# Kernel tuning notes

Hardware: AMD Instinct MI355X
Metric: run time of the kernel (lower is better)

## Reference

```python
import jax, jax.numpy as jnp
import numpy as np
import math

WS = 7  # window size
NUM_HEADS = 6

def _relative_position_index(ws):
    coords = np.stack(np.meshgrid(np.arange(ws), np.arange(ws), indexing='ij'))  # 2,ws,ws
    cf = coords.reshape(2, -1)
    rel = cf[:, :, None] - cf[:, None, :]            # 2,N,N
    rel = rel.transpose(1, 2, 0).astype(np.int64)    # N,N,2
    rel[:, :, 0] += ws - 1
    rel[:, :, 1] += ws - 1
    rel[:, :, 0] *= 2 * ws - 1
    return jnp.asarray(rel.sum(-1))                  # N,N

RPI = _relative_position_index(WS)

def setup_inputs() -> dict:
    key = jax.random.key(0)
    ks = jax.random.split(key, 6)
    C = 192
    return {
        'x': jax.random.normal(ks[0], (32, 3136, C), dtype=jnp.float32),
        'gamma': jnp.ones((C,), dtype=jnp.float32),
        'rpb_table': jax.random.normal(ks[1], (169, NUM_HEADS), dtype=jnp.float32) * 0.02,
        'qkv_w': jax.random.normal(ks[2], (3 * C, C), dtype=jnp.float32) * (1.0 / math.sqrt(C)),
        'qkv_b': jax.random.normal(ks[3], (3 * C,), dtype=jnp.float32) * 0.02,
        'proj_w': jax.random.normal(ks[4], (C, C), dtype=jnp.float32) * (1.0 / math.sqrt(C)),
        'proj_b': jax.random.normal(ks[5], (C,), dtype=jnp.float32) * 0.02,
    }

def reference(x, gamma, rpb_table, qkv_w, qkv_b, proj_w, proj_b):
    B_, N, C = x.shape
    H = W = int(math.isqrt(N))
    h = NUM_HEADS
    d = C // h
    scale = d ** -0.5
    ws = WS
    NW = ws * ws  # tokens per window (49)

    # LayerNorm (beta = 0)
    mu = jnp.mean(x, axis=-1, keepdims=True)
    var = jnp.var(x, axis=-1, keepdims=True)
    xn = (x - mu) * jax.lax.rsqrt(var + 1e-5) * gamma

    # window partition: (B_,H,W,C) -> (B_*nWh*nWw, ws*ws, C)
    xn = xn.reshape(B_, H // ws, ws, W // ws, ws, C)
    xw = xn.transpose(0, 1, 3, 2, 4, 5).reshape(-1, NW, C)
    BW = xw.shape[0]

    # qkv projection
    qkv = xw @ qkv_w.T + qkv_b                        # (BW, NW, 3C)
    qkv = qkv.reshape(BW, NW, 3, h, d).transpose(2, 0, 3, 1, 4)
    q, k, v = qkv[0], qkv[1], qkv[2]                  # (BW, h, NW, d)

    attn = jnp.einsum('bhnd,bhmd->bhnm', q * scale, k)
    bias = rpb_table[RPI.reshape(-1)].reshape(NW, NW, h).transpose(2, 0, 1)
    attn = jax.nn.softmax(attn + bias[None], axis=-1)

    out = jnp.einsum('bhnm,bhmd->bhnd', attn, v)      # (BW, h, NW, d)
    out = out.transpose(0, 2, 1, 3).reshape(BW, NW, C)
    out = out @ proj_w.T + proj_b

    # window reverse
    out = out.reshape(B_, H // ws, W // ws, ws, ws, C)
    out = out.transpose(0, 1, 3, 2, 4, 5).reshape(B_, H * W, C)
    return out
```

## Files before the change

### kernel.cpp

```cpp
#include <hip/hip_runtime.h>


typedef __bf16 bf16x8 __attribute__((ext_vector_type(8)));
typedef float  f32x4  __attribute__((ext_vector_type(4)));
typedef unsigned int u32;
union U128 { uint4 u; bf16x8 v; };

__device__ __forceinline__ f32x4 mfma16(bf16x8 a, bf16x8 b, f32x4 c){
  return __builtin_amdgcn_mfma_f32_16x16x32_bf16(a, b, c, 0, 0, 0);
}
__device__ __forceinline__ f32x4 f4zero(){
  f32x4 z; z[0]=0.f; z[1]=0.f; z[2]=0.f; z[3]=0.f; return z;
}
__device__ __forceinline__ unsigned short f2bf(float f){
  union{float f; unsigned int i;} x; x.f = f;
  unsigned int r = x.i + 0x7fffu + ((x.i >> 16) & 1u);
  return (unsigned short)(r >> 16);
}
__device__ __forceinline__ bf16x8 ldfrag(const unsigned short* p){
  U128 x; x.u = *(const uint4*)p; return x.v;
}
__device__ __forceinline__ int div7(int t){ return (t * 9363) >> 16; }

__device__ __forceinline__ void glds16(const unsigned short* g, unsigned short* l){
  __builtin_amdgcn_global_load_lds((const __attribute__((address_space(1))) u32*)g,
                                   (__attribute__((address_space(3))) u32*)l, 16, 0, 0);
}

__global__ __launch_bounds__(256, 8) void wa_ln(
    const float* __restrict__ x, const float* __restrict__ gamma,
    unsigned short* __restrict__ xng,
    const float* __restrict__ qkv_w, const float* __restrict__ proj_w,
    const float* __restrict__ rpb,
    unsigned short* __restrict__ wq, unsigned short* __restrict__ wp,
    float* __restrict__ bt)
{
  const int tid  = threadIdx.x;

  if (blockIdx.x < 432){
    int i = blockIdx.x * 256 + tid;
    if (i < 576*192) wq[i] = f2bf(qkv_w[i]);
    if (i < 192*192) wp[i] = f2bf(proj_w[i]);
    if (i < 6*64*64){
      int head = i >> 12, t = (i >> 6) & 63, j = i & 63;
      int l16 = j >> 2, nt = j & 3;
      int col = nt*16 + l16;
      float v;
      if (t < 49 && col < 49){
        int tr = div7(t),   tc = t   - tr*7;
        int jr = div7(col), jc = col - jr*7;
        v = rpb[((tr - jr + 6)*13 + (tc - jc + 6))*6 + head];
      } else {
        v = (col >= 49) ? -3.0e38f : 0.0f;
      }
      bt[i] = v;
    }
  }

  const int wave = tid >> 6, lane = tid & 63;
  const int wid  = blockIdx.x * 4 + wave;
  const int wi   = wid >> 6, t = wid & 63;
  unsigned short* dst = xng + (size_t)wid * 192;
  if (t >= 49){
    if (lane < 24){ const uint4 z = {0u,0u,0u,0u}; *(uint4*)&dst[lane*8] = z; }
    return;
  }
  const int b = wi >> 6, wr = (wi >> 3) & 7, wc = wi & 7;
  const int tr = div7(t), tc = t - tr*7;
  const float* xt = x + ((size_t)b*3136 + (size_t)((wr*7 + tr)*56 + wc*7 + tc)) * 192;
  float v0 = xt[lane], v1 = xt[lane+64], v2 = xt[lane+128];
  float s  = v0 + v1 + v2;
  float sq = v0*v0 + v1*v1 + v2*v2;
#pragma unroll
  for (int off = 32; off > 0; off >>= 1){
    s  += __shfl_xor(s,  off);
    sq += __shfl_xor(sq, off);
  }
  float mu  = s * (1.0f/192.0f);
  float var = sq * (1.0f/192.0f) - mu*mu;
  float inv = rsqrtf(var + 1e-5f);
  const int sw = (t & 7) << 3;
  dst[lane        ^ sw] = f2bf((v0 - mu)*inv*gamma[lane]);
  dst[(lane + 64) ^ sw] = f2bf((v1 - mu)*inv*gamma[lane+64]);
  dst[(lane + 128)^ sw] = f2bf((v2 - mu)*inv*gamma[lane+128]);
}

__global__ __launch_bounds__(384, 5) void wa_k1(
    const unsigned short* __restrict__ xng, const float* __restrict__ bt,
    const unsigned short* __restrict__ wq, const float* __restrict__ qkv_b,
    unsigned short* __restrict__ attn)
{
  __shared__ __align__(16) unsigned short qk[3*64*72];
  __shared__ __align__(16) unsigned short xnb[64*192];

  const int p    = blockIdx.x;
  const int blk  = (p & 7) * 512 + (p >> 3);
  const int wi   = blk >> 1;
  const int h0   = (blk & 1) * 3;
  const int b    = wi >> 6;
  const int wr   = (wi >> 3) & 7;
  const int wc   = wi & 7;
  const int tid  = threadIdx.x;
  const int wave = tid >> 6;
  const int lane = tid & 63;
  const int quad = lane >> 4;
  const int l16  = lane & 15;

  {
    const unsigned short* xw = xng + (size_t)wi * 64 * 192;
#pragma unroll
    for (int j = 0; j < 4; j++){
      const int chunk = wave*4 + j;
      glds16(xw + chunk*512 + lane*8, &xnb[chunk*512]);
    }
  }
  __syncthreads();

  f32x4 acc[4][3];
  {
    const int sec = wave >> 1;
    const int n0  = sec*192 + h0*32 + (wave & 1)*48;
#pragma unroll
    for (int mt = 0; mt < 4; mt++)
#pragma unroll
      for (int nt = 0; nt < 3; nt++) acc[mt][nt] = f4zero();

#pragma unroll
    for (int kt = 0; kt < 6; kt++){
      bf16x8 a[4], bw[3];
#pragma unroll
      for (int nt = 0; nt < 3; nt++)
        bw[nt] = ldfrag(&wq[(size_t)(n0 + nt*16 + l16)*192 + kt*32 + quad*8]);
#pragma unroll
      for (int mt = 0; mt < 4; mt++)
        a[mt] = ldfrag(&xnb[(mt*16 + l16)*192 + ((kt*32 + quad*8) ^ ((l16 & 7) << 3))]);
#pragma unroll
      for (int mt = 0; mt < 4; mt++)
#pragma unroll
        for (int nt = 0; nt < 3; nt++)
          acc[mt][nt] = mfma16(a[mt], bw[nt], acc[mt][nt]);
    }
  }
  __syncthreads();

  unsigned short* const vt = xnb;
  {
    const int sec = wave >> 1;
    const int n0  = sec*192 + h0*32 + (wave & 1)*48;
    const float scale = 0.17677669529663687f;
#pragma unroll
    for (int nt = 0; nt < 3; nt++){
      const int bc = (wave & 1)*48 + nt*16 + l16;
      const int hl2 = bc >> 5, d = bc & 31;
      const float bias = qkv_b[n0 + nt*16 + l16];
#pragma unroll
      for (int mt = 0; mt < 4; mt++)
#pragma unroll
        for (int r = 0; r < 4; r++){
          const int row = mt*16 + quad*4 + r;
          const float val = acc[mt][nt][r] + bias;
          if (sec == 0)      qk[(hl2*64 + row)*72 + d]      = f2bf(val * scale);
          else if (sec == 1) qk[(hl2*64 + row)*72 + 32 + d] = f2bf(val);
          else               vt[(hl2*32 + d)*72 + row]      = f2bf(val);
        }
    }
  }
  __syncthreads();

  const int hl   = wave >> 1;
  const int half = wave & 1;
  const int head = h0 + hl;

  f32x4 bias4[2][4];
#pragma unroll
  for (int i = 0; i < 2; i++)
#pragma unroll
    for (int r = 0; r < 4; r++){
      const int t = half*32 + i*16 + quad*4 + r;
      bias4[i][r] = *(const f32x4*)&bt[head*4096 + t*64 + l16*4];
    }

  bf16x8 aq[2];
#pragma unroll
  for (int i = 0; i < 2; i++)
    aq[i] = ldfrag(&qk[(hl*64 + half*32 + i*16 + l16)*72 + quad*8]);

  f32x4 s[2][4];
#pragma unroll
  for (int nt = 0; nt < 4; nt++){
    bf16x8 bk = ldfrag(&qk[(hl*64 + nt*16 + l16)*72 + 32 + quad*8]);
#pragma unroll
    for (int i = 0; i < 2; i++)
      s[i][nt] = mfma16(aq[i], bk, f4zero());
  }

  __syncthreads();

  float linv[2][4];
#pragma unroll
  for (int i = 0; i < 2; i++)
#pragma unroll
    for (int r = 0; r < 4; r++){
      const f32x4 b4 = bias4[i][r];
#pragma unroll
      for (int nt = 0; nt < 4; nt++) s[i][nt][r] += b4[nt];
      float m = fmaxf(fmaxf(s[i][0][r], s[i][1][r]), fmaxf(s[i][2][r], s[i][3][r]));
#pragma unroll
      for (int off = 8; off > 0; off >>= 1) m = fmaxf(m, __shfl_xor(m, off));
      float l = 0.f;
      const int t = half*32 + i*16 + quad*4 + r;
#pragma unroll
      for (int nt = 0; nt < 4; nt++){
        float pexp = __expf(s[i][nt][r] - m);
        l += pexp;
        qk[hl*4608 + t*72 + nt*16 + l16] = f2bf(pexp);
      }
#pragma unroll
      for (int off = 8; off > 0; off >>= 1) l += __shfl_xor(l, off);
      linv[i][r] = 1.f / l;
    }

  f32x4 o[2][2];
#pragma unroll
  for (int i = 0; i < 2; i++)
#pragma unroll
    for (int n2 = 0; n2 < 2; n2++) o[i][n2] = f4zero();
#pragma unroll
  for (int kt = 0; kt < 2; kt++){
    bf16x8 ap[2], bv[2];
#pragma unroll
    for (int i = 0; i < 2; i++)
      ap[i] = ldfrag(&qk[hl*4608 + (half*32 + i*16 + l16)*72 + kt*32 + quad*8]);
#pragma unroll
    for (int n2 = 0; n2 < 2; n2++)
      bv[n2] = ldfrag(&vt[(hl*32 + n2*16 + l16)*72 + kt*32 + quad*8]);
#pragma unroll
    for (int i = 0; i < 2; i++)
#pragma unroll
      for (int n2 = 0; n2 < 2; n2++)
        o[i][n2] = mfma16(ap[i], bv[n2], o[i][n2]);
  }

#pragma unroll
  for (int i = 0; i < 2; i++)
#pragma unroll
    for (int r = 0; r < 4; r++){
      const int t = half*32 + i*16 + quad*4 + r;
      if (t < 49){
        const int tr = div7(t), tcc = t - tr*7;
        const size_t base =
          ((size_t)b*3136 + (size_t)((wr*7 + tr)*56 + wc*7 + tcc))*192 + head*32;
        const float inv = linv[i][r];
        attn[base + l16]      = f2bf(o[i][0][r] * inv);
        attn[base + 16 + l16] = f2bf(o[i][1][r] * inv);
      }
    }
}

__global__ __launch_bounds__(256, 4) void wa_k2(
    const unsigned short* __restrict__ a, const unsigned short* __restrict__ wp,
    const float* __restrict__ pb, float* __restrict__ out)
{
  const int mblk = blockIdx.x;
  const int nblk = blockIdx.y;
  const int tid  = threadIdx.x;
  const int wave = tid >> 6;
  const int lane = tid & 63;
  const int quad = lane >> 4;
  const int l16  = lane & 15;

  bf16x8 av[6][2];
#pragma unroll
  for (int kt = 0; kt < 6; kt++)
#pragma unroll
    for (int i = 0; i < 2; i++)
      av[kt][i] = ldfrag(&a[(size_t)(mblk*128 + (wave*2 + i)*16 + l16)*192 + kt*32 + quad*8]);
  __builtin_amdgcn_sched_barrier(0);

  f32x4 acc[2][4];
#pragma unroll
  for (int i = 0; i < 2; i++)
#pragma unroll
    for (int nt = 0; nt < 4; nt++) acc[i][nt] = f4zero();

#pragma unroll
  for (int kt = 0; kt < 6; kt++){
    bf16x8 bw[4];
#pragma unroll
    for (int nt = 0; nt < 4; nt++)
      bw[nt] = ldfrag(&wp[(size_t)(nblk*64 + nt*16 + l16)*192 + kt*32 + quad*8]);
#pragma unroll
    for (int i = 0; i < 2; i++)
#pragma unroll
      for (int nt = 0; nt < 4; nt++)
        acc[i][nt] = mfma16(av[kt][i], bw[nt], acc[i][nt]);
  }

#pragma unroll
  for (int nt = 0; nt < 4; nt++){
    const int col = nblk*64 + nt*16 + l16;
    const float bias = pb[col];
#pragma unroll
    for (int i = 0; i < 2; i++)
#pragma unroll
      for (int r = 0; r < 4; r++){
        const int row = mblk*128 + (wave*2 + i)*16 + quad*4 + r;
        out[(size_t)row*192 + col] = acc[i][nt][r] + bias;
      }
  }
}

extern "C" void kernel_launch(void* const* d_in, const int* in_sizes, int n_in,
                              void* d_out, int out_size, void* d_ws, size_t ws_size,
                              hipStream_t stream) {
  (void)in_sizes; (void)n_in; (void)out_size; (void)ws_size;
  const float* x      = (const float*)d_in[0];
  const float* gamma  = (const float*)d_in[1];
  const float* rpb    = (const float*)d_in[2];
  const float* qkv_w  = (const float*)d_in[3];
  const float* qkv_b  = (const float*)d_in[4];
  const float* proj_w = (const float*)d_in[5];
  const float* proj_b = (const float*)d_in[6];

  unsigned short* wq   = (unsigned short*)d_ws;
  unsigned short* wp   = wq + 576*192;
  float* bt            = (float*)(wp + 192*192);
  unsigned short* attn = (unsigned short*)(bt + 6*64*64);

  unsigned short* xng = (unsigned short*)d_out;
  float* out = (float*)d_out;

  hipLaunchKernelGGL(wa_ln, dim3(32768), dim3(256), 0, stream,
                     x, gamma, xng, qkv_w, proj_w, rpb, wq, wp, bt);
  hipLaunchKernelGGL(wa_k1, dim3(4096), dim3(384), 0, stream,
                     xng, bt, wq, qkv_b, attn);
  hipLaunchKernelGGL(wa_k2, dim3(784, 3), dim3(256), 0, stream,
                     attn, wp, proj_b, out);
}
```

Measured before the change: 306.0 us.

## Fuse output projection into window attention kernel, one block per window

The attention kernel now processes all six heads of a window in one block. It does them in two rounds of three heads, interleaving the QKV GEMM of the next round with attention. It then applies the output projection on the attention result kept in LDS, so the separate projection kernel and the bf16 attention round-trip through global memory go away. The LayerNorm kernel now runs one block per window and stores the normalized tokens compactly (49 rows) in workspace instead of padded 64 rows in the output buffer, and the attention kernel zero-pads in LDS. This trades more LDS and registers per block and lower occupancy (launch bound 3) for less global traffic and one fewer launch.

```diff
diff --git a/kernel.cpp b/kernel.cpp
--- a/kernel.cpp
+++ b/kernel.cpp
@@ -35,7 +35,7 @@
     unsigned short* __restrict__ wq, unsigned short* __restrict__ wp,
     float* __restrict__ bt)
 {
-  const int tid  = threadIdx.x;
+  const int tid = threadIdx.x;
 
   if (blockIdx.x < 432){
     int i = blockIdx.x * 256 + tid;
@@ -58,45 +58,45 @@
   }
 
   const int wave = tid >> 6, lane = tid & 63;
-  const int wid  = blockIdx.x * 4 + wave;
-  const int wi   = wid >> 6, t = wid & 63;
-  unsigned short* dst = xng + (size_t)wid * 192;
-  if (t >= 49){
-    if (lane < 24){ const uint4 z = {0u,0u,0u,0u}; *(uint4*)&dst[lane*8] = z; }
-    return;
+  const int wi = blockIdx.x;
+  const int b = wi >> 6, wrr = (wi >> 3) & 7, wcc = wi & 7;
+  const float g0 = gamma[lane], g1 = gamma[lane+64], g2 = gamma[lane+128];
+  const float* xb = x + (size_t)b * 3136 * 192;
+
+  for (int t = wave; t < 49; t += 4){
+    const int tr = div7(t), tc = t - tr*7;
+    const float* xt = xb + (size_t)((wrr*7 + tr)*56 + wcc*7 + tc) * 192;
+    float v0 = xt[lane], v1 = xt[lane+64], v2 = xt[lane+128];
+    float s  = v0 + v1 + v2;
+    float sq = v0*v0 + v1*v1 + v2*v2;
+#pragma unroll
+    for (int off = 32; off > 0; off >>= 1){
+      s  += __shfl_xor(s,  off);
+      sq += __shfl_xor(sq, off);
+    }
+    float mu  = s * (1.0f/192.0f);
+    float var = sq * (1.0f/192.0f) - mu*mu;
+    float inv = rsqrtf(var + 1e-5f);
+    unsigned short* dst = xng + ((size_t)wi*49 + t) * 192;
+    const int sw = (t & 7) << 3;
+    dst[lane        ^ sw] = f2bf((v0 - mu)*inv*g0);
+    dst[(lane + 64) ^ sw] = f2bf((v1 - mu)*inv*g1);
+    dst[(lane + 128)^ sw] = f2bf((v2 - mu)*inv*g2);
   }
-  const int b = wi >> 6, wr = (wi >> 3) & 7, wc = wi & 7;
-  const int tr = div7(t), tc = t - tr*7;
-  const float* xt = x + ((size_t)b*3136 + (size_t)((wr*7 + tr)*56 + wc*7 + tc)) * 192;
-  float v0 = xt[lane], v1 = xt[lane+64], v2 = xt[lane+128];
-  float s  = v0 + v1 + v2;
-  float sq = v0*v0 + v1*v1 + v2*v2;
-#pragma unroll
-  for (int off = 32; off > 0; off >>= 1){
-    s  += __shfl_xor(s,  off);
-    sq += __shfl_xor(sq, off);
-  }
-  float mu  = s * (1.0f/192.0f);
-  float var = sq * (1.0f/192.0f) - mu*mu;
-  float inv = rsqrtf(var + 1e-5f);
-  const int sw = (t & 7) << 3;
-  dst[lane        ^ sw] = f2bf((v0 - mu)*inv*gamma[lane]);
-  dst[(lane + 64) ^ sw] = f2bf((v1 - mu)*inv*gamma[lane+64]);
-  dst[(lane + 128)^ sw] = f2bf((v2 - mu)*inv*gamma[lane+128]);
-}
-
-__global__ __launch_bounds__(384, 5) void wa_k1(
+}
+
+#define OBS 104
+__global__ __launch_bounds__(384, 3) void wa_k1(
     const unsigned short* __restrict__ xng, const float* __restrict__ bt,
     const unsigned short* __restrict__ wq, const float* __restrict__ qkv_b,
-    unsigned short* __restrict__ attn)
+    const unsigned short* __restrict__ wp, const float* __restrict__ pb,
+    float* __restrict__ out)
 {
   __shared__ __align__(16) unsigned short qk[3*64*72];
+  __shared__ __align__(16) unsigned short vt[3*32*72];
   __shared__ __align__(16) unsigned short xnb[64*192];
 
-  const int p    = blockIdx.x;
-  const int blk  = (p & 7) * 512 + (p >> 3);
-  const int wi   = blk >> 1;
-  const int h0   = (blk & 1) * 3;
+  const int wi   = blockIdx.x;
   const int b    = wi >> 6;
   const int wr   = (wi >> 3) & 7;
   const int wc   = wi & 7;
@@ -105,26 +105,35 @@
   const int lane = tid & 63;
   const int quad = lane >> 4;
   const int l16  = lane & 15;
-
+  const int sec  = wave >> 1, sub = wave & 1;
+  const int hl   = wave >> 1, half = wave & 1;
+
+  unsigned short* const ob = xnb;
+
+  const float pbv0 = pb[wave*32 + l16];
+  const float pbv1 = pb[wave*32 + 16 + l16];
+
+  const unsigned short* xw = xng + (size_t)wi * 49 * 192;
   {
-    const unsigned short* xw = xng + (size_t)wi * 64 * 192;
-#pragma unroll
-    for (int j = 0; j < 4; j++){
-      const int chunk = wave*4 + j;
+    const uint4 z = {0u,0u,0u,0u};
+    for (int i = tid; i < 360; i += 384) *(uint4*)&xnb[9408 + i*8] = z;
+    uint4 r48;
+    if (tid < 24) r48 = *(const uint4*)(xw + 9216 + tid*8);
+#pragma unroll
+    for (int j = 0; j < 3; j++){
+      const int chunk = wave*3 + j;
       glds16(xw + chunk*512 + lane*8, &xnb[chunk*512]);
     }
+    if (tid < 24) *(uint4*)&xnb[9216 + tid*8] = r48;
   }
   __syncthreads();
 
-  f32x4 acc[4][3];
-  {
-    const int sec = wave >> 1;
-    const int n0  = sec*192 + h0*32 + (wave & 1)*48;
+  auto qkv_gemm = [&](f32x4 (*acc)[3], int np){
+    const int n0 = sec*192 + np*96 + sub*48;
 #pragma unroll
     for (int mt = 0; mt < 4; mt++)
 #pragma unroll
       for (int nt = 0; nt < 3; nt++) acc[mt][nt] = f4zero();
-
 #pragma unroll
     for (int kt = 0; kt < 6; kt++){
       bf16x8 a[4], bw[3];
@@ -140,17 +149,14 @@
         for (int nt = 0; nt < 3; nt++)
           acc[mt][nt] = mfma16(a[mt], bw[nt], acc[mt][nt]);
     }
-  }
-  __syncthreads();
-
-  unsigned short* const vt = xnb;
-  {
-    const int sec = wave >> 1;
-    const int n0  = sec*192 + h0*32 + (wave & 1)*48;
+  };
+
+  auto qkv_epi = [&](f32x4 (*acc)[3], int np){
+    const int n0 = sec*192 + np*96 + sub*48;
     const float scale = 0.17677669529663687f;
 #pragma unroll
     for (int nt = 0; nt < 3; nt++){
-      const int bc = (wave & 1)*48 + nt*16 + l16;
+      const int bc = sub*48 + nt*16 + l16;
       const int hl2 = bc >> 5, d = bc & 31;
       const float bias = qkv_b[n0 + nt*16 + l16];
 #pragma unroll
@@ -164,148 +170,147 @@
           else               vt[(hl2*32 + d)*72 + row]      = f2bf(val);
         }
     }
-  }
-  __syncthreads();
-
-  const int hl   = wave >> 1;
-  const int half = wave & 1;
-  const int head = h0 + hl;
-
-  f32x4 bias4[2][4];
-#pragma unroll
-  for (int i = 0; i < 2; i++)
-#pragma unroll
-    for (int r = 0; r < 4; r++){
-      const int t = half*32 + i*16 + quad*4 + r;
-      bias4[i][r] = *(const f32x4*)&bt[head*4096 + t*64 + l16*4];
-    }
-
-  bf16x8 aq[2];
-#pragma unroll
-  for (int i = 0; i < 2; i++)
-    aq[i] = ldfrag(&qk[(hl*64 + half*32 + i*16 + l16)*72 + quad*8]);
-
-  f32x4 s[2][4];
-#pragma unroll
-  for (int nt = 0; nt < 4; nt++){
-    bf16x8 bk = ldfrag(&qk[(hl*64 + nt*16 + l16)*72 + 32 + quad*8]);
-#pragma unroll
-    for (int i = 0; i < 2; i++)
-      s[i][nt] = mfma16(aq[i], bk, f4zero());
-  }
-
-  __syncthreads();
-
-  float linv[2][4];
-#pragma unroll
-  for (int i = 0; i < 2; i++)
-#pragma unroll
-    for (int r = 0; r < 4; r++){
-      const f32x4 b4 = bias4[i][r];
-#pragma unroll
-      for (int nt = 0; nt < 4; nt++) s[i][nt][r] += b4[nt];
-      float m = fmaxf(fmaxf(s[i][0][r], s[i][1][r]), fmaxf(s[i][2][r], s[i][3][r]));
-#pragma unroll
-      for (int off = 8; off > 0; off >>= 1) m = fmaxf(m, __shfl_xor(m, off));
-      float l = 0.f;
-      const int t = half*32 + i*16 + quad*4 + r;
-#pragma unroll
-      for (int nt = 0; nt < 4; nt++){
-        float pexp = __expf(s[i][nt][r] - m);
-        l += pexp;
-        qk[hl*4608 + t*72 + nt*16 + l16] = f2bf(pexp);
-      }
-#pragma unroll
-      for (int off = 8; off > 0; off >>= 1) l += __shfl_xor(l, off);
-      linv[i][r] = 1.f / l;
-    }
-
-  f32x4 o[2][2];
-#pragma unroll
-  for (int i = 0; i < 2; i++)
-#pragma unroll
-    for (int n2 = 0; n2 < 2; n2++) o[i][n2] = f4zero();
-#pragma unroll
-  for (int kt = 0; kt < 2; kt++){
-    bf16x8 ap[2], bv[2];
-#pragma unroll
-    for (int i = 0; i < 2; i++)
-      ap[i] = ldfrag(&qk[hl*4608 + (half*32 + i*16 + l16)*72 + kt*32 + quad*8]);
-#pragma unroll
-    for (int n2 = 0; n2 < 2; n2++)
-      bv[n2] = ldfrag(&vt[(hl*32 + n2*16 + l16)*72 + kt*32 + quad*8]);
-#pragma unroll
-    for (int i = 0; i < 2; i++)
+  };
+
+  auto attn_round = [&](int np){
+    const int head = np*3 + hl;
+    f32x4 bias4[2][4];
+#pragma unroll
+    for (int i = 0; i < 2; i++)
+#pragma unroll
+      for (int r = 0; r < 4; r++){
+        const int t = half*32 + i*16 + quad*4 + r;
+        bias4[i][r] = *(const f32x4*)&bt[head*4096 + t*64 + l16*4];
+      }
+
+    bf16x8 aq[2];
+#pragma unroll
+    for (int i = 0; i < 2; i++)
+      aq[i] = ldfrag(&qk[(hl*64 + half*32 + i*16 + l16)*72 + quad*8]);
+
+    f32x4 s[2][4];
+#pragma unroll
+    for (int nt = 0; nt < 4; nt++){
+      bf16x8 bk = ldfrag(&qk[(hl*64 + nt*16 + l16)*72 + 32 + quad*8]);
+#pragma unroll
+      for (int i = 0; i < 2; i++)
+        s[i][nt] = mfma16(aq[i], bk, f4zero());
+    }
+
+    __syncthreads();
+
+    float linv[2][4];
+#pragma unroll
+    for (int i = 0; i < 2; i++)
+#pragma unroll
+      for (int r = 0; r < 4; r++){
+        const f32x4 b4 = bias4[i][r];
+#pragma unroll
+        for (int nt = 0; nt < 4; nt++) s[i][nt][r] += b4[nt];
+        float m = fmaxf(fmaxf(s[i][0][r], s[i][1][r]), fmaxf(s[i][2][r], s[i][3][r]));
+#pragma unroll
+        for (int off = 8; off > 0; off >>= 1) m = fmaxf(m, __shfl_xor(m, off));
+        float l = 0.f;
+        const int t = half*32 + i*16 + quad*4 + r;
+#pragma unroll
+        for (int nt = 0; nt < 4; nt++){
+          float pexp = __expf(s[i][nt][r] - m);
+          l += pexp;
+          qk[hl*4608 + t*72 + nt*16 + l16] = f2bf(pexp);
+        }
+#pragma unroll
+        for (int off = 8; off > 0; off >>= 1) l += __shfl_xor(l, off);
+        linv[i][r] = 1.f / l;
+      }
+
+    f32x4 o[2][2];
+#pragma unroll
+    for (int i = 0; i < 2; i++)
+#pragma unroll
+      for (int n2 = 0; n2 < 2; n2++) o[i][n2] = f4zero();
+#pragma unroll
+    for (int kt = 0; kt < 2; kt++){
+      bf16x8 ap[2], bv[2];
+#pragma unroll
+      for (int i = 0; i < 2; i++)
+        ap[i] = ldfrag(&qk[hl*4608 + (half*32 + i*16 + l16)*72 + kt*32 + quad*8]);
 #pragma unroll
       for (int n2 = 0; n2 < 2; n2++)
-        o[i][n2] = mfma16(ap[i], bv[n2], o[i][n2]);
-  }
-
-#pragma unroll
-  for (int i = 0; i < 2; i++)
-#pragma unroll
-    for (int r = 0; r < 4; r++){
-      const int t = half*32 + i*16 + quad*4 + r;
-      if (t < 49){
-        const int tr = div7(t), tcc = t - tr*7;
-        const size_t base =
-          ((size_t)b*3136 + (size_t)((wr*7 + tr)*56 + wc*7 + tcc))*192 + head*32;
+        bv[n2] = ldfrag(&vt[(hl*32 + n2*16 + l16)*72 + kt*32 + quad*8]);
+#pragma unroll
+      for (int i = 0; i < 2; i++)
+#pragma unroll
+        for (int n2 = 0; n2 < 2; n2++)
+          o[i][n2] = mfma16(ap[i], bv[n2], o[i][n2]);
+    }
+
+#pragma unroll
+    for (int i = 0; i < 2; i++)
+#pragma unroll
+      for (int r = 0; r < 4; r++){
+        const int t = half*32 + i*16 + quad*4 + r;
         const float inv = linv[i][r];
-        attn[base + l16]      = f2bf(o[i][0][r] * inv);
-        attn[base + 16 + l16] = f2bf(o[i][1][r] * inv);
-      }
-    }
-}
-
-__global__ __launch_bounds__(256, 4) void wa_k2(
-    const unsigned short* __restrict__ a, const unsigned short* __restrict__ wp,
-    const float* __restrict__ pb, float* __restrict__ out)
-{
-  const int mblk = blockIdx.x;
-  const int nblk = blockIdx.y;
-  const int tid  = threadIdx.x;
-  const int wave = tid >> 6;
-  const int lane = tid & 63;
-  const int quad = lane >> 4;
-  const int l16  = lane & 15;
-
-  bf16x8 av[6][2];
-#pragma unroll
-  for (int kt = 0; kt < 6; kt++)
-#pragma unroll
-    for (int i = 0; i < 2; i++)
-      av[kt][i] = ldfrag(&a[(size_t)(mblk*128 + (wave*2 + i)*16 + l16)*192 + kt*32 + quad*8]);
-  __builtin_amdgcn_sched_barrier(0);
-
-  f32x4 acc[2][4];
-#pragma unroll
-  for (int i = 0; i < 2; i++)
-#pragma unroll
-    for (int nt = 0; nt < 4; nt++) acc[i][nt] = f4zero();
-
-#pragma unroll
-  for (int kt = 0; kt < 6; kt++){
-    bf16x8 bw[4];
-#pragma unroll
-    for (int nt = 0; nt < 4; nt++)
-      bw[nt] = ldfrag(&wp[(size_t)(nblk*64 + nt*16 + l16)*192 + kt*32 + quad*8]);
-#pragma unroll
-    for (int i = 0; i < 2; i++)
-#pragma unroll
-      for (int nt = 0; nt < 4; nt++)
-        acc[i][nt] = mfma16(av[kt][i], bw[nt], acc[i][nt]);
-  }
-
-#pragma unroll
-  for (int nt = 0; nt < 4; nt++){
-    const int col = nblk*64 + nt*16 + l16;
-    const float bias = pb[col];
-#pragma unroll
-    for (int i = 0; i < 2; i++)
+        ob[t*OBS + hl*32 + l16]      = f2bf(o[i][0][r] * inv);
+        ob[t*OBS + hl*32 + 16 + l16] = f2bf(o[i][1][r] * inv);
+      }
+  };
+
+  auto proj_part = [&](f32x4 (*pacc)[2], int np){
+#pragma unroll
+    for (int kt = 0; kt < 3; kt++){
+      bf16x8 a2[4], bw2[2];
+#pragma unroll
+      for (int n2 = 0; n2 < 2; n2++)
+        bw2[n2] = ldfrag(&wp[(size_t)(wave*32 + n2*16 + l16)*192 + np*96 + kt*32 + quad*8]);
+#pragma unroll
+      for (int mt = 0; mt < 4; mt++)
+        a2[mt] = ldfrag(&ob[(mt*16 + l16)*OBS + kt*32 + quad*8]);
+#pragma unroll
+      for (int mt = 0; mt < 4; mt++)
+#pragma unroll
+        for (int n2 = 0; n2 < 2; n2++)
+          pacc[mt][n2] = mfma16(a2[mt], bw2[n2], pacc[mt][n2]);
+    }
+  };
+
+  f32x4 acc0[4][3], acc1[4][3];
+  qkv_gemm(acc0, 0);
+  qkv_epi (acc0, 0);
+  qkv_gemm(acc1, 1);
+  __syncthreads();
+
+  attn_round(0);
+  __syncthreads();
+
+  qkv_epi(acc1, 1);
+  f32x4 pacc[4][2];
+#pragma unroll
+  for (int mt = 0; mt < 4; mt++)
+#pragma unroll
+    for (int n2 = 0; n2 < 2; n2++) pacc[mt][n2] = f4zero();
+  proj_part(pacc, 0);
+  __syncthreads();
+
+  attn_round(1);
+  __syncthreads();
+
+  proj_part(pacc, 1);
+
+#pragma unroll
+  for (int n2 = 0; n2 < 2; n2++){
+    const float bias = n2 ? pbv1 : pbv0;
+#pragma unroll
+    for (int mt = 0; mt < 4; mt++)
 #pragma unroll
       for (int r = 0; r < 4; r++){
-        const int row = mblk*128 + (wave*2 + i)*16 + quad*4 + r;
-        out[(size_t)row*192 + col] = acc[i][nt][r] + bias;
+        const int t = mt*16 + quad*4 + r;
+        if (t < 49){
+          const int tr = div7(t), tcc = t - tr*7;
+          const size_t base =
+            ((size_t)b*3136 + (size_t)((wr*7 + tr)*56 + wc*7 + tcc))*192
+            + wave*32 + n2*16 + l16;
+          out[base] = pacc[mt][n2][r] + bias;
+        }
       }
   }
 }
@@ -322,18 +327,14 @@
   const float* proj_w = (const float*)d_in[5];
   const float* proj_b = (const float*)d_in[6];
 
-  unsigned short* wq   = (unsigned short*)d_ws;
-  unsigned short* wp   = wq + 576*192;
-  float* bt            = (float*)(wp + 192*192);
-  unsigned short* attn = (unsigned short*)(bt + 6*64*64);
-
-  unsigned short* xng = (unsigned short*)d_out;
+  unsigned short* wq  = (unsigned short*)d_ws;
+  unsigned short* wp  = wq + 576*192;
+  float* bt           = (float*)(wp + 192*192);
+  unsigned short* xng = (unsigned short*)(bt + 6*64*64);
   float* out = (float*)d_out;
 
-  hipLaunchKernelGGL(wa_ln, dim3(32768), dim3(256), 0, stream,
+  hipLaunchKernelGGL(wa_ln, dim3(2048), dim3(256), 0, stream,
                      x, gamma, xng, qkv_w, proj_w, rpb, wq, wp, bt);
-  hipLaunchKernelGGL(wa_k1, dim3(4096), dim3(384), 0, stream,
-                     xng, bt, wq, qkv_b, attn);
-  hipLaunchKernelGGL(wa_k2, dim3(784, 3), dim3(256), 0, stream,
-                     attn, wp, proj_b, out);
-}
+  hipLaunchKernelGGL(wa_k1, dim3(2048), dim3(384), 0, stream,
+                     xng, bt, wq, qkv_b, wp, proj_b, out);
+}
```

After: 419.3 us. 1.37x slower.
